# Kernel optimization log

Measured on AMD Instinct MI355X. Metric: run time of the kernel, lower is better.

The kernel has to match this reference:

```python
import jax, jax.numpy as jnp
import numpy as np

N_NODES = 50000
N_EDGES = 1600000
IN_FEATS = 256
OUT_FEATS = 64


def setup_inputs() -> dict:
    key = jax.random.key(0)
    k_x, k_w, k_b, k_s, k_d = jax.random.split(key, 5)
    x = jax.random.normal(k_x, (N_NODES, IN_FEATS), dtype=jnp.float32)
    # nn.Linear(in_feats, out_feats): weight [out, in], bias [out]
    W = jax.random.normal(k_w, (OUT_FEATS, IN_FEATS), dtype=jnp.float32) / np.sqrt(IN_FEATS)
    b = jax.random.normal(k_b, (OUT_FEATS,), dtype=jnp.float32) * 0.01
    edge_src = jax.random.randint(k_s, (N_EDGES,), 0, N_NODES, dtype=jnp.int32)
    edge_dst = jax.random.randint(k_d, (N_EDGES,), 0, N_NODES, dtype=jnp.int32)
    return {"x": x, "W": W, "b": b, "edge_src": edge_src, "edge_dst": edge_dst}


def reference(x, W, b, edge_src, edge_dst):
    # h = dropout(relu(Linear(x)))  -- dropout p=0 (eval) => identity
    h = jax.nn.relu(x @ W.T + b)                     # [N, out_feats]
    # update_all: message = h[src], reduce = mean over incoming edges per dst
    msg = h[edge_src]                                # [E, out_feats] gather
    summed = jax.ops.segment_sum(msg, edge_dst, num_segments=N_NODES)  # [N, out]
    deg = jax.ops.segment_sum(jnp.ones((edge_src.shape[0],), dtype=h.dtype),
                              edge_dst, num_segments=N_NODES)          # [N]
    deg = jnp.maximum(deg, 1.0)
    return summed / deg[:, None]
```

## Files before the change

### kernel.cpp

```cpp
#include <hip/hip_runtime.h>
#include <hip/hip_bf16.h>

#define K_IN 256
#define O_OUT 64
#define NBINS 1024
#define NPB 49
#define CAP 1824
#define PART_CHUNK 4096

typedef __attribute__((ext_vector_type(8))) short short8;
typedef __attribute__((ext_vector_type(4))) float f32x4;
typedef __attribute__((ext_vector_type(2))) unsigned u32x2;
typedef __attribute__((ext_vector_type(4))) unsigned u32x4;

#define GLOAD4(dst, base, voff, imm)                                     \
  asm volatile("global_load_dwordx4 %0, %1, %2 offset:" #imm             \
               : "=v"(dst) : "v"(voff), "s"(base))
#define GLOAD2(dst, base, voff)                                          \
  asm volatile("global_load_dwordx2 %0, %1, %2"                          \
               : "=v"(dst) : "v"(voff), "s"(base))
__device__ inline void vmwait0() {
  asm volatile("s_waitcnt vmcnt(0)" ::: "memory");
  __builtin_amdgcn_sched_barrier(0);
}

__device__ inline unsigned short bf16bits(float a) {
  __hip_bfloat16 t = __float2bfloat16(a);
  return *(unsigned short*)&t;
}

__device__ inline short8 cvt8u(u32x4 lo, u32x4 hi) {
  short8 r;
  r[0] = (short)bf16bits(__uint_as_float(lo[0]));
  r[1] = (short)bf16bits(__uint_as_float(lo[1]));
  r[2] = (short)bf16bits(__uint_as_float(lo[2]));
  r[3] = (short)bf16bits(__uint_as_float(lo[3]));
  r[4] = (short)bf16bits(__uint_as_float(hi[0]));
  r[5] = (short)bf16bits(__uint_as_float(hi[1]));
  r[6] = (short)bf16bits(__uint_as_float(hi[2]));
  r[7] = (short)bf16bits(__uint_as_float(hi[3]));
  return r;
}

__global__ __launch_bounds__(256) void k_prep(const float* __restrict__ W,
                                              unsigned short* __restrict__ Wb,
                                              int* __restrict__ cursor) {
  int i = blockIdx.x * 256 + threadIdx.x;
  Wb[i] = bf16bits(W[i]);
  if (i < NBINS) cursor[i] = 0;
}

struct GemmSmem {
  unsigned short wsb[64 * 256];
};
struct PartSmem {
  int cnt[NBINS];
  int scanb[NBINS];
  int gbase[NBINS];
  int wsum[4];
  unsigned ord[PART_CHUNK];
};
union FusedSmem {
  GemmSmem g;
  PartSmem p;
};

__device__ void gemm_body(GemmSmem& sm, int gid, const float* __restrict__ x,
                          const unsigned short* __restrict__ Wb,
                          const float* __restrict__ bias,
                          __hip_bfloat16* __restrict__ h, int N) {
  const int tid = threadIdx.x;
  const int lane = tid & 63;
  const int wv = tid >> 6;
  const int n0 = gid * 64;

  int anode = n0 + wv * 16 + (lane & 15);
  if (anode > N - 1) anode = N - 1;
  unsigned voff = (unsigned)anode * (K_IN * 4) + (unsigned)((lane >> 4) * 32);

  u32x4 f[16];
  GLOAD4(f[0], x, voff, 0);    GLOAD4(f[1], x, voff, 16);
  GLOAD4(f[2], x, voff, 128);  GLOAD4(f[3], x, voff, 144);
  GLOAD4(f[4], x, voff, 256);  GLOAD4(f[5], x, voff, 272);
  GLOAD4(f[6], x, voff, 384);  GLOAD4(f[7], x, voff, 400);
  GLOAD4(f[8], x, voff, 512);  GLOAD4(f[9], x, voff, 528);
  GLOAD4(f[10], x, voff, 640); GLOAD4(f[11], x, voff, 656);
  GLOAD4(f[12], x, voff, 768); GLOAD4(f[13], x, voff, 784);
  GLOAD4(f[14], x, voff, 896); GLOAD4(f[15], x, voff, 912);
  __builtin_amdgcn_sched_barrier(0);

  {
    const uint4* wsrc = (const uint4*)Wb;
#pragma unroll
    for (int r = 0; r < 8; ++r) {
      uint4 w = wsrc[r * 256 + tid];
      int flat = r * 256 + tid;
      int row = flat >> 5;
      int c16 = flat & 31;
      unsigned byte = (unsigned)(row * 512 + c16 * 16);
      byte ^= (unsigned)((row & 7) << 4);
      *(uint4*)((char*)sm.wsb + byte) = w;
    }
  }
  __syncthreads();
  vmwait0();

  const int brow0 = lane & 15;
  const unsigned kb = (unsigned)((lane >> 4) * 16);
  const unsigned bswz = (unsigned)((brow0 & 7) << 4);

  f32x4 acc[4] = {{0.f, 0.f, 0.f, 0.f}, {0.f, 0.f, 0.f, 0.f},
                  {0.f, 0.f, 0.f, 0.f}, {0.f, 0.f, 0.f, 0.f}};
#pragma unroll
  for (int k8 = 0; k8 < 8; ++k8) {
    short8 a = cvt8u(f[2 * k8], f[2 * k8 + 1]);
#pragma unroll
    for (int nt = 0; nt < 4; ++nt) {
      unsigned byte = (unsigned)((brow0 + nt * 16) * 512 + k8 * 64) + kb;
      byte ^= bswz;
      short8 bfr = *(const short8*)((const char*)sm.wsb + byte);
      acc[nt] = __builtin_amdgcn_mfma_f32_16x16x32_bf16(a, bfr, acc[nt], 0, 0, 0);
    }
  }

  const int col = lane & 15;
  const int rbase = (lane >> 4) * 4;
#pragma unroll
  for (int nt = 0; nt < 4; ++nt) {
    float bv = bias[nt * 16 + col];
#pragma unroll
    for (int j = 0; j < 4; ++j) {
      int node = n0 + wv * 16 + rbase + j;
      if (node < N) {
        float v = fmaxf(acc[nt][j] + bv, 0.f);
        h[(size_t)node * O_OUT + nt * 16 + col] = __float2bfloat16(v);
      }
    }
  }
}

__device__ void part_body(PartSmem& sm, int pid, const int* __restrict__ esrc,
                          const int* __restrict__ edst, int* __restrict__ cursor,
                          unsigned* __restrict__ bucket, int E) {
  const int tid = threadIdx.x;
  const int lane = tid & 63;
  const int wid = tid >> 6;
  const int base = pid * PART_CHUNK;

  u32x4 s4[4], d4[4];
  unsigned vo[4];
#pragma unroll
  for (int r = 0; r < 4; ++r) {
    int e0 = base + r * 1024 + tid * 4;
    if (e0 > E - 4) e0 = E - 4;
    vo[r] = (unsigned)e0 * 4u;
  }
  GLOAD4(s4[0], esrc, vo[0], 0); GLOAD4(d4[0], edst, vo[0], 0);
  GLOAD4(s4[1], esrc, vo[1], 0); GLOAD4(d4[1], edst, vo[1], 0);
  GLOAD4(s4[2], esrc, vo[2], 0); GLOAD4(d4[2], edst, vo[2], 0);
  GLOAD4(s4[3], esrc, vo[3], 0); GLOAD4(d4[3], edst, vo[3], 0);
  __builtin_amdgcn_sched_barrier(0);

#pragma unroll
  for (int r = 0; r < 4; ++r) sm.cnt[r * 256 + tid] = 0;
  __syncthreads();
  vmwait0();

  unsigned pk[16];
  int rk[16];
#pragma unroll
  for (int r = 0; r < 4; ++r) {
#pragma unroll
    for (int j = 0; j < 4; ++j) {
      int k = r * 4 + j;
      int e = base + r * 1024 + tid * 4 + j;
      if (e < E) {
        int d = (int)d4[r][j];
        int bb = (int)__umulhi((unsigned)d, 87652394u);
        int dl = d - bb * NPB;
        pk[k] = (s4[r][j] & 0xFFFFu) | ((unsigned)dl << 16) | ((unsigned)bb << 22);
        rk[k] = atomicAdd(&sm.cnt[bb], 1);
      } else {
        rk[k] = -1;
      }
    }
  }
  __syncthreads();

  int c0 = sm.cnt[4 * tid];
  int c1 = sm.cnt[4 * tid + 1];
  int c2 = sm.cnt[4 * tid + 2];
  int c3 = sm.cnt[4 * tid + 3];
  int s = c0 + c1 + c2 + c3;
  int incl = s;
#pragma unroll
  for (int off = 1; off < 64; off <<= 1) {
    int t = __shfl_up(incl, off);
    if (lane >= off) incl += t;
  }
  if (lane == 63) sm.wsum[wid] = incl;
  __syncthreads();
  int wpre = 0;
  for (int w = 0; w < wid; ++w) wpre += sm.wsum[w];
  int excl = wpre + incl - s;
  sm.scanb[4 * tid] = excl;
  sm.scanb[4 * tid + 1] = excl + c0;
  sm.scanb[4 * tid + 2] = excl + c0 + c1;
  sm.scanb[4 * tid + 3] = excl + c0 + c1 + c2;
  sm.gbase[4 * tid] = (c0 > 0) ? atomicAdd(&cursor[4 * tid], c0) : 0;
  sm.gbase[4 * tid + 1] = (c1 > 0) ? atomicAdd(&cursor[4 * tid + 1], c1) : 0;
  sm.gbase[4 * tid + 2] = (c2 > 0) ? atomicAdd(&cursor[4 * tid + 2], c2) : 0;
  sm.gbase[4 * tid + 3] = (c3 > 0) ? atomicAdd(&cursor[4 * tid + 3], c3) : 0;
  __syncthreads();

#pragma unroll
  for (int k = 0; k < 16; ++k) {
    if (rk[k] >= 0) {
      int bb = (int)(pk[k] >> 22);
      int pos = sm.scanb[bb] + rk[k];
      sm.ord[pos] = pk[k];
    }
  }
  __syncthreads();

  int nv = E - base;
  if (nv > PART_CHUNK) nv = PART_CHUNK;
  for (int p = tid; p < nv; p += 256) {
    unsigned v = sm.ord[p];
    int bb = v >> 22;
    int slot = sm.gbase[bb] + (p - sm.scanb[bb]);
    if (slot < CAP) bucket[(size_t)bb * CAP + slot] = v;
  }
}

__global__ __launch_bounds__(256, 4) void k_fused(const float* __restrict__ x,
                                                  const unsigned short* __restrict__ Wb,
                                                  const float* __restrict__ bias,
                                                  __hip_bfloat16* __restrict__ h,
                                                  const int* __restrict__ esrc,
                                                  const int* __restrict__ edst,
                                                  int* __restrict__ cursor,
                                                  unsigned* __restrict__ bucket,
                                                  int N, int E) {
  __shared__ FusedSmem sm;
  const int npart = (E + PART_CHUNK - 1) / PART_CHUNK;
  const int b = blockIdx.x;
  if (b % 3 == 1 && b / 3 < npart) {
    part_body(sm.p, b / 3, esrc, edst, cursor, bucket, E);
  } else {
    int skipped = (b + 2) / 3;
    if (skipped > npart) skipped = npart;
    gemm_body(sm.g, b - skipped, x, Wb, bias, h, N);
  }
}

__global__ __launch_bounds__(256, 4) void k_sortagg(const unsigned* __restrict__ bucket,
                                                    const int* __restrict__ cursor,
                                                    const unsigned* __restrict__ h32,
                                                    float* __restrict__ out, int N) {
  __shared__ int hist[NPB];
  __shared__ int offs[NPB];
  __shared__ unsigned short sbuf[CAP + 64];

  const int tid = threadIdx.x;
  const int lane = tid & 63;
  const int wid = tid >> 6;
  const int bin = blockIdx.x;

  if (tid < NPB) hist[tid] = 0;
  __syncthreads();

  int cnt = cursor[bin];
  if (cnt > CAP) cnt = CAP;
  const unsigned* bb = bucket + (size_t)bin * CAP;

  unsigned pk2[2][4];
  int rk2[2][4];
#pragma unroll
  for (int g = 0; g < 2; ++g) {
    int i0 = (g * 256 + tid) * 4;
    uint4 v;
    if (i0 + 3 < cnt) {
      v = *(const uint4*)(bb + i0);
    } else {
      v = make_uint4(0, 0, 0, 0);
      unsigned* vp = (unsigned*)&v;
      for (int j = 0; j < 4; ++j)
        if (i0 + j < cnt) vp[j] = bb[i0 + j];
    }
    const unsigned* vp = (const unsigned*)&v;
#pragma unroll
    for (int j = 0; j < 4; ++j) {
      if (i0 + j < cnt) {
        pk2[g][j] = vp[j];
        rk2[g][j] = atomicAdd(&hist[(vp[j] >> 16) & 63], 1);
      } else {
        rk2[g][j] = -1;
      }
    }
  }
  __syncthreads();

  if (tid < 64) {
    int hval = (tid < NPB) ? hist[tid] : 0;
    int incl = hval;
#pragma unroll
    for (int off = 1; off < 64; off <<= 1) {
      int t = __shfl_up(incl, off);
      if (lane >= off) incl += t;
    }
    if (tid < NPB) offs[tid] = incl - hval;
  }
  __syncthreads();

#pragma unroll
  for (int g = 0; g < 2; ++g)
#pragma unroll
    for (int j = 0; j < 4; ++j)
      if (rk2[g][j] >= 0)
        sbuf[offs[(pk2[g][j] >> 16) & 63] + rk2[g][j]] =
            (unsigned short)(pk2[g][j] & 0xFFFFu);
  __syncthreads();

  const int q = lane >> 4;
  const int hl = lane & 15;
  const unsigned hlb = (unsigned)hl * 8u;

  for (int nl = wid; nl < NPB; nl += 8) {
    const int nlb = nl + 4;
    const bool hasb = (nlb < NPB);
    const int ca = hist[nl];
    const int cb = hasb ? hist[nlb] : 0;
    const unsigned short* bsa = sbuf + offs[nl];
    const unsigned short* bsb = sbuf + (hasb ? offs[nlb] : 0);

    unsigned voa[12], vob[12];
#pragma unroll
    for (int k = 0; k < 12; ++k) {
      int e = k * 4 + q;
      unsigned pa = (e < ca) ? (unsigned)bsa[e] : 0u;
      unsigned pb = (e < cb) ? (unsigned)bsb[e] : 0u;
      voa[k] = pa * 128u + hlb;
      vob[k] = pb * 128u + hlb;
    }
    u32x2 ua[12], ub[12];
#pragma unroll
    for (int k = 0; k < 12; ++k) { GLOAD2(ua[k], h32, voa[k]); }
#pragma unroll
    for (int k = 0; k < 12; ++k) { GLOAD2(ub[k], h32, vob[k]); }
    vmwait0();

    float a0 = 0.f, a1 = 0.f, a2 = 0.f, a3 = 0.f;
    float b0 = 0.f, b1 = 0.f, b2 = 0.f, b3 = 0.f;
#pragma unroll
    for (int k = 0; k < 12; ++k) {
      float wk = (k * 4 + q < ca) ? 1.f : 0.f;
      a0 = fmaf(wk, __uint_as_float(ua[k][0] << 16), a0);
      a1 = fmaf(wk, __uint_as_float(ua[k][0] & 0xFFFF0000u), a1);
      a2 = fmaf(wk, __uint_as_float(ua[k][1] << 16), a2);
      a3 = fmaf(wk, __uint_as_float(ua[k][1] & 0xFFFF0000u), a3);
    }
#pragma unroll
    for (int k = 0; k < 12; ++k) {
      float wk = (k * 4 + q < cb) ? 1.f : 0.f;
      b0 = fmaf(wk, __uint_as_float(ub[k][0] << 16), b0);
      b1 = fmaf(wk, __uint_as_float(ub[k][0] & 0xFFFF0000u), b1);
      b2 = fmaf(wk, __uint_as_float(ub[k][1] << 16), b2);
      b3 = fmaf(wk, __uint_as_float(ub[k][1] & 0xFFFF0000u), b3);
    }

    const uint2* __restrict__ h2 = (const uint2*)h32;
    for (int e0 = 48; e0 < ca; e0 += 4) {
      int e = e0 + q;
      float wk = (e < ca) ? 1.f : 0.f;
      int p = (e < ca) ? (int)bsa[e] : 0;
      uint2 u = h2[(size_t)p * 16 + hl];
      a0 = fmaf(wk, __uint_as_float(u.x << 16), a0);
      a1 = fmaf(wk, __uint_as_float(u.x & 0xFFFF0000u), a1);
      a2 = fmaf(wk, __uint_as_float(u.y << 16), a2);
      a3 = fmaf(wk, __uint_as_float(u.y & 0xFFFF0000u), a3);
    }
    for (int e0 = 48; e0 < cb; e0 += 4) {
      int e = e0 + q;
      float wk = (e < cb) ? 1.f : 0.f;
      int p = (e < cb) ? (int)bsb[e] : 0;
      uint2 u = h2[(size_t)p * 16 + hl];
      b0 = fmaf(wk, __uint_as_float(u.x << 16), b0);
      b1 = fmaf(wk, __uint_as_float(u.x & 0xFFFF0000u), b1);
      b2 = fmaf(wk, __uint_as_float(u.y << 16), b2);
      b3 = fmaf(wk, __uint_as_float(u.y & 0xFFFF0000u), b3);
    }

    a0 += __shfl_xor(a0, 16); a1 += __shfl_xor(a1, 16);
    a2 += __shfl_xor(a2, 16); a3 += __shfl_xor(a3, 16);
    b0 += __shfl_xor(b0, 16); b1 += __shfl_xor(b1, 16);
    b2 += __shfl_xor(b2, 16); b3 += __shfl_xor(b3, 16);
    a0 += __shfl_xor(a0, 32); a1 += __shfl_xor(a1, 32);
    a2 += __shfl_xor(a2, 32); a3 += __shfl_xor(a3, 32);
    b0 += __shfl_xor(b0, 32); b1 += __shfl_xor(b1, 32);
    b2 += __shfl_xor(b2, 32); b3 += __shfl_xor(b3, 32);

    if (lane < 16) {
      int na = bin * NPB + nl;
      if (na < N) {
        float inv = 1.f / fmaxf((float)ca, 1.f);
        float4 r;
        r.x = a0 * inv; r.y = a1 * inv; r.z = a2 * inv; r.w = a3 * inv;
        *(float4*)(out + (size_t)na * O_OUT + hl * 4) = r;
      }
      int nb = bin * NPB + nlb;
      if (hasb && nb < N) {
        float inv = 1.f / fmaxf((float)cb, 1.f);
        float4 r;
        r.x = b0 * inv; r.y = b1 * inv; r.z = b2 * inv; r.w = b3 * inv;
        *(float4*)(out + (size_t)nb * O_OUT + hl * 4) = r;
      }
    }
  }
}

extern "C" void kernel_launch(void* const* d_in, const int* in_sizes, int n_in,
                              void* d_out, int out_size, void* d_ws, size_t ws_size,
                              hipStream_t stream) {
  const float* x = (const float*)d_in[0];
  const float* W = (const float*)d_in[1];
  const float* b = (const float*)d_in[2];
  const int* esrc = (const int*)d_in[3];
  const int* edst = (const int*)d_in[4];
  float* out = (float*)d_out;

  const int N = in_sizes[0] / K_IN;
  const int E = in_sizes[3];

  char* ws = (char*)d_ws;
  unsigned short* Wb = (unsigned short*)ws;
  __hip_bfloat16* h = (__hip_bfloat16*)(ws + 32768);
  size_t off = 32768 + (size_t)N * O_OUT * sizeof(__hip_bfloat16);
  int* cursor = (int*)(ws + off);
  off += NBINS * sizeof(int);
  unsigned* bucket = (unsigned*)(ws + off);

  const int ngemm = (N + 63) / 64;
  const int npart = (E + PART_CHUNK - 1) / PART_CHUNK;

  k_prep<<<(K_IN * O_OUT) / 256, 256, 0, stream>>>(W, Wb, cursor);
  k_fused<<<ngemm + npart, 256, 0, stream>>>(x, Wb, b, h, esrc, edst, cursor,
                                             bucket, N, E);
  k_sortagg<<<NBINS, 256, 0, stream>>>(bucket, cursor, (const unsigned*)h, out, N);
}
```

Measured before the change: 160.7 us.

## Shrink LDS use: GEMM reads W from global, halve partition chunk, raise occupancy

The GEMM path stops staging the bf16 weight matrix in LDS and reads B fragments straight from global/L2. It also drops the hand-issued asm loads in favour of plain float4 loads. The partition chunk is halved to 2048 edges and the count and scan arrays are merged, so the fused kernel's shared memory shrinks. Blocks now alternate strictly between GEMM and partition roles, and launch bounds ask for 8 blocks per CU. The aim is higher occupancy and better latency hiding, at the cost of repeated global reads of W, twice as many partition blocks, and more global cursor atomics.

```diff
diff --git a/kernel.cpp b/kernel.cpp
--- a/kernel.cpp
+++ b/kernel.cpp
@@ -6,16 +6,12 @@
 #define NBINS 1024
 #define NPB 49
 #define CAP 1824
-#define PART_CHUNK 4096
+#define PART_CHUNK 2048
 
 typedef __attribute__((ext_vector_type(8))) short short8;
 typedef __attribute__((ext_vector_type(4))) float f32x4;
 typedef __attribute__((ext_vector_type(2))) unsigned u32x2;
-typedef __attribute__((ext_vector_type(4))) unsigned u32x4;
-
-#define GLOAD4(dst, base, voff, imm)                                     \
-  asm volatile("global_load_dwordx4 %0, %1, %2 offset:" #imm             \
-               : "=v"(dst) : "v"(voff), "s"(base))
+
 #define GLOAD2(dst, base, voff)                                          \
   asm volatile("global_load_dwordx2 %0, %1, %2"                          \
                : "=v"(dst) : "v"(voff), "s"(base))
@@ -29,16 +25,12 @@
   return *(unsigned short*)&t;
 }
 
-__device__ inline short8 cvt8u(u32x4 lo, u32x4 hi) {
+__device__ inline short8 cvt8(float4 f0, float4 f1) {
   short8 r;
-  r[0] = (short)bf16bits(__uint_as_float(lo[0]));
-  r[1] = (short)bf16bits(__uint_as_float(lo[1]));
-  r[2] = (short)bf16bits(__uint_as_float(lo[2]));
-  r[3] = (short)bf16bits(__uint_as_float(lo[3]));
-  r[4] = (short)bf16bits(__uint_as_float(hi[0]));
-  r[5] = (short)bf16bits(__uint_as_float(hi[1]));
-  r[6] = (short)bf16bits(__uint_as_float(hi[2]));
-  r[7] = (short)bf16bits(__uint_as_float(hi[3]));
+  r[0] = (short)bf16bits(f0.x); r[1] = (short)bf16bits(f0.y);
+  r[2] = (short)bf16bits(f0.z); r[3] = (short)bf16bits(f0.w);
+  r[4] = (short)bf16bits(f1.x); r[5] = (short)bf16bits(f1.y);
+  r[6] = (short)bf16bits(f1.z); r[7] = (short)bf16bits(f1.w);
   return r;
 }
 
@@ -50,22 +42,14 @@
   if (i < NBINS) cursor[i] = 0;
 }
 
-struct GemmSmem {
-  unsigned short wsb[64 * 256];
-};
 struct PartSmem {
-  int cnt[NBINS];
-  int scanb[NBINS];
+  int cntscan[NBINS];
   int gbase[NBINS];
   int wsum[4];
   unsigned ord[PART_CHUNK];
 };
-union FusedSmem {
-  GemmSmem g;
-  PartSmem p;
-};
-
-__device__ void gemm_body(GemmSmem& sm, int gid, const float* __restrict__ x,
+
+__device__ void gemm_body(int gid, const float* __restrict__ x,
                           const unsigned short* __restrict__ Wb,
                           const float* __restrict__ bias,
                           __hip_bfloat16* __restrict__ h, int N) {
@@ -76,49 +60,19 @@
 
   int anode = n0 + wv * 16 + (lane & 15);
   if (anode > N - 1) anode = N - 1;
-  unsigned voff = (unsigned)anode * (K_IN * 4) + (unsigned)((lane >> 4) * 32);
-
-  u32x4 f[16];
-  GLOAD4(f[0], x, voff, 0);    GLOAD4(f[1], x, voff, 16);
-  GLOAD4(f[2], x, voff, 128);  GLOAD4(f[3], x, voff, 144);
-  GLOAD4(f[4], x, voff, 256);  GLOAD4(f[5], x, voff, 272);
-  GLOAD4(f[6], x, voff, 384);  GLOAD4(f[7], x, voff, 400);
-  GLOAD4(f[8], x, voff, 512);  GLOAD4(f[9], x, voff, 528);
-  GLOAD4(f[10], x, voff, 640); GLOAD4(f[11], x, voff, 656);
-  GLOAD4(f[12], x, voff, 768); GLOAD4(f[13], x, voff, 784);
-  GLOAD4(f[14], x, voff, 896); GLOAD4(f[15], x, voff, 912);
-  __builtin_amdgcn_sched_barrier(0);
-
-  {
-    const uint4* wsrc = (const uint4*)Wb;
-#pragma unroll
-    for (int r = 0; r < 8; ++r) {
-      uint4 w = wsrc[r * 256 + tid];
-      int flat = r * 256 + tid;
-      int row = flat >> 5;
-      int c16 = flat & 31;
-      unsigned byte = (unsigned)(row * 512 + c16 * 16);
-      byte ^= (unsigned)((row & 7) << 4);
-      *(uint4*)((char*)sm.wsb + byte) = w;
-    }
-  }
-  __syncthreads();
-  vmwait0();
-
-  const int brow0 = lane & 15;
-  const unsigned kb = (unsigned)((lane >> 4) * 16);
-  const unsigned bswz = (unsigned)((brow0 & 7) << 4);
+  const float* aptr = x + (size_t)anode * K_IN + (lane >> 4) * 8;
+  const unsigned short* bptr = Wb + (lane & 15) * K_IN + (lane >> 4) * 8;
 
   f32x4 acc[4] = {{0.f, 0.f, 0.f, 0.f}, {0.f, 0.f, 0.f, 0.f},
                   {0.f, 0.f, 0.f, 0.f}, {0.f, 0.f, 0.f, 0.f}};
 #pragma unroll
   for (int k8 = 0; k8 < 8; ++k8) {
-    short8 a = cvt8u(f[2 * k8], f[2 * k8 + 1]);
+    float4 f0 = *(const float4*)(aptr + k8 * 32);
+    float4 f1 = *(const float4*)(aptr + k8 * 32 + 4);
+    short8 a = cvt8(f0, f1);
 #pragma unroll
     for (int nt = 0; nt < 4; ++nt) {
-      unsigned byte = (unsigned)((brow0 + nt * 16) * 512 + k8 * 64) + kb;
-      byte ^= bswz;
-      short8 bfr = *(const short8*)((const char*)sm.wsb + byte);
+      short8 bfr = *(const short8*)(bptr + nt * 16 * K_IN + k8 * 32);
       acc[nt] = __builtin_amdgcn_mfma_f32_16x16x32_bf16(a, bfr, acc[nt], 0, 0, 0);
     }
   }
@@ -147,39 +101,36 @@
   const int wid = tid >> 6;
   const int base = pid * PART_CHUNK;
 
-  u32x4 s4[4], d4[4];
-  unsigned vo[4];
-#pragma unroll
-  for (int r = 0; r < 4; ++r) {
+#pragma unroll
+  for (int r = 0; r < 4; ++r) sm.cntscan[r * 256 + tid] = 0;
+
+  int4 s4[2], d4[2];
+#pragma unroll
+  for (int r = 0; r < 2; ++r) {
     int e0 = base + r * 1024 + tid * 4;
     if (e0 > E - 4) e0 = E - 4;
-    vo[r] = (unsigned)e0 * 4u;
-  }
-  GLOAD4(s4[0], esrc, vo[0], 0); GLOAD4(d4[0], edst, vo[0], 0);
-  GLOAD4(s4[1], esrc, vo[1], 0); GLOAD4(d4[1], edst, vo[1], 0);
-  GLOAD4(s4[2], esrc, vo[2], 0); GLOAD4(d4[2], edst, vo[2], 0);
-  GLOAD4(s4[3], esrc, vo[3], 0); GLOAD4(d4[3], edst, vo[3], 0);
-  __builtin_amdgcn_sched_barrier(0);
-
-#pragma unroll
-  for (int r = 0; r < 4; ++r) sm.cnt[r * 256 + tid] = 0;
-  __syncthreads();
-  vmwait0();
-
-  unsigned pk[16];
-  int rk[16];
-#pragma unroll
-  for (int r = 0; r < 4; ++r) {
+    s4[r] = *(const int4*)(esrc + e0);
+    d4[r] = *(const int4*)(edst + e0);
+  }
+  __syncthreads();
+
+  unsigned pk[8];
+  int rk[8];
+#pragma unroll
+  for (int r = 0; r < 2; ++r) {
+    const int* sp = (const int*)&s4[r];
+    const int* dp = (const int*)&d4[r];
 #pragma unroll
     for (int j = 0; j < 4; ++j) {
       int k = r * 4 + j;
       int e = base + r * 1024 + tid * 4 + j;
       if (e < E) {
-        int d = (int)d4[r][j];
+        int d = dp[j];
         int bb = (int)__umulhi((unsigned)d, 87652394u);
         int dl = d - bb * NPB;
-        pk[k] = (s4[r][j] & 0xFFFFu) | ((unsigned)dl << 16) | ((unsigned)bb << 22);
-        rk[k] = atomicAdd(&sm.cnt[bb], 1);
+        pk[k] = ((unsigned)sp[j] & 0xFFFFu) | ((unsigned)dl << 16) |
+                ((unsigned)bb << 22);
+        rk[k] = atomicAdd(&sm.cntscan[bb], 1);
       } else {
         rk[k] = -1;
       }
@@ -187,10 +138,10 @@
   }
   __syncthreads();
 
-  int c0 = sm.cnt[4 * tid];
-  int c1 = sm.cnt[4 * tid + 1];
-  int c2 = sm.cnt[4 * tid + 2];
-  int c3 = sm.cnt[4 * tid + 3];
+  int c0 = sm.cntscan[4 * tid];
+  int c1 = sm.cntscan[4 * tid + 1];
+  int c2 = sm.cntscan[4 * tid + 2];
+  int c3 = sm.cntscan[4 * tid + 3];
   int s = c0 + c1 + c2 + c3;
   int incl = s;
 #pragma unroll
@@ -203,10 +154,10 @@
   int wpre = 0;
   for (int w = 0; w < wid; ++w) wpre += sm.wsum[w];
   int excl = wpre + incl - s;
-  sm.scanb[4 * tid] = excl;
-  sm.scanb[4 * tid + 1] = excl + c0;
-  sm.scanb[4 * tid + 2] = excl + c0 + c1;
-  sm.scanb[4 * tid + 3] = excl + c0 + c1 + c2;
+  sm.cntscan[4 * tid] = excl;
+  sm.cntscan[4 * tid + 1] = excl + c0;
+  sm.cntscan[4 * tid + 2] = excl + c0 + c1;
+  sm.cntscan[4 * tid + 3] = excl + c0 + c1 + c2;
   sm.gbase[4 * tid] = (c0 > 0) ? atomicAdd(&cursor[4 * tid], c0) : 0;
   sm.gbase[4 * tid + 1] = (c1 > 0) ? atomicAdd(&cursor[4 * tid + 1], c1) : 0;
   sm.gbase[4 * tid + 2] = (c2 > 0) ? atomicAdd(&cursor[4 * tid + 2], c2) : 0;
@@ -214,11 +165,10 @@
   __syncthreads();
 
 #pragma unroll
-  for (int k = 0; k < 16; ++k) {
+  for (int k = 0; k < 8; ++k) {
     if (rk[k] >= 0) {
       int bb = (int)(pk[k] >> 22);
-      int pos = sm.scanb[bb] + rk[k];
-      sm.ord[pos] = pk[k];
+      sm.ord[sm.cntscan[bb] + rk[k]] = pk[k];
     }
   }
   __syncthreads();
@@ -228,12 +178,12 @@
   for (int p = tid; p < nv; p += 256) {
     unsigned v = sm.ord[p];
     int bb = v >> 22;
-    int slot = sm.gbase[bb] + (p - sm.scanb[bb]);
+    int slot = sm.gbase[bb] + (p - sm.cntscan[bb]);
     if (slot < CAP) bucket[(size_t)bb * CAP + slot] = v;
   }
 }
 
-__global__ __launch_bounds__(256, 4) void k_fused(const float* __restrict__ x,
+__global__ __launch_bounds__(256, 8) void k_fused(const float* __restrict__ x,
                                                   const unsigned short* __restrict__ Wb,
                                                   const float* __restrict__ bias,
                                                   __hip_bfloat16* __restrict__ h,
@@ -242,16 +192,10 @@
                                                   int* __restrict__ cursor,
                                                   unsigned* __restrict__ bucket,
                                                   int N, int E) {
-  __shared__ FusedSmem sm;
-  const int npart = (E + PART_CHUNK - 1) / PART_CHUNK;
+  __shared__ PartSmem sm;
   const int b = blockIdx.x;
-  if (b % 3 == 1 && b / 3 < npart) {
-    part_body(sm.p, b / 3, esrc, edst, cursor, bucket, E);
-  } else {
-    int skipped = (b + 2) / 3;
-    if (skipped > npart) skipped = npart;
-    gemm_body(sm.g, b - skipped, x, Wb, bias, h, N);
-  }
+  if (b & 1) part_body(sm, b >> 1, esrc, edst, cursor, bucket, E);
+  else gemm_body(b >> 1, x, Wb, bias, h, N);
 }
 
 __global__ __launch_bounds__(256, 4) void k_sortagg(const unsigned* __restrict__ bucket,
```

Result: slower. 189.6 us (+17.9%).

## Stage x tile through LDS as bf16 and drop inline-asm loads

Applied to the files above, without the earlier changes.

The GEMM part no longer keeps the whole x row fragment in 16 vector registers loaded by inline asm. It loads x cooperatively with coalesced float4 reads, converts to bf16, writes a swizzled tile into a new LDS buffer, and reads MFMA A-fragments from LDS. The partition part switches from asm loads to plain int4 loads with a scalar tail path. Launch bounds drop to 2 blocks per CU, and LDS per block doubles for the GEMM layout. Coalescing improves and register pressure falls, but occupancy drops and the early overlap of x loads with the W staging is lost.

```diff
diff --git a/kernel.cpp b/kernel.cpp
--- a/kernel.cpp
+++ b/kernel.cpp
@@ -11,11 +11,7 @@
 typedef __attribute__((ext_vector_type(8))) short short8;
 typedef __attribute__((ext_vector_type(4))) float f32x4;
 typedef __attribute__((ext_vector_type(2))) unsigned u32x2;
-typedef __attribute__((ext_vector_type(4))) unsigned u32x4;
-
-#define GLOAD4(dst, base, voff, imm)                                     \
-  asm volatile("global_load_dwordx4 %0, %1, %2 offset:" #imm             \
-               : "=v"(dst) : "v"(voff), "s"(base))
+
 #define GLOAD2(dst, base, voff)                                          \
   asm volatile("global_load_dwordx2 %0, %1, %2"                          \
                : "=v"(dst) : "v"(voff), "s"(base))
@@ -29,16 +25,12 @@
   return *(unsigned short*)&t;
 }
 
-__device__ inline short8 cvt8u(u32x4 lo, u32x4 hi) {
+__device__ inline short8 cvt8(float4 f0, float4 f1) {
   short8 r;
-  r[0] = (short)bf16bits(__uint_as_float(lo[0]));
-  r[1] = (short)bf16bits(__uint_as_float(lo[1]));
-  r[2] = (short)bf16bits(__uint_as_float(lo[2]));
-  r[3] = (short)bf16bits(__uint_as_float(lo[3]));
-  r[4] = (short)bf16bits(__uint_as_float(hi[0]));
-  r[5] = (short)bf16bits(__uint_as_float(hi[1]));
-  r[6] = (short)bf16bits(__uint_as_float(hi[2]));
-  r[7] = (short)bf16bits(__uint_as_float(hi[3]));
+  r[0] = (short)bf16bits(f0.x); r[1] = (short)bf16bits(f0.y);
+  r[2] = (short)bf16bits(f0.z); r[3] = (short)bf16bits(f0.w);
+  r[4] = (short)bf16bits(f1.x); r[5] = (short)bf16bits(f1.y);
+  r[6] = (short)bf16bits(f1.z); r[7] = (short)bf16bits(f1.w);
   return r;
 }
 
@@ -52,6 +44,7 @@
 
 struct GemmSmem {
   unsigned short wsb[64 * 256];
+  unsigned short xs[64 * 256];
 };
 struct PartSmem {
   int cnt[NBINS];
@@ -74,21 +67,6 @@
   const int wv = tid >> 6;
   const int n0 = gid * 64;
 
-  int anode = n0 + wv * 16 + (lane & 15);
-  if (anode > N - 1) anode = N - 1;
-  unsigned voff = (unsigned)anode * (K_IN * 4) + (unsigned)((lane >> 4) * 32);
-
-  u32x4 f[16];
-  GLOAD4(f[0], x, voff, 0);    GLOAD4(f[1], x, voff, 16);
-  GLOAD4(f[2], x, voff, 128);  GLOAD4(f[3], x, voff, 144);
-  GLOAD4(f[4], x, voff, 256);  GLOAD4(f[5], x, voff, 272);
-  GLOAD4(f[6], x, voff, 384);  GLOAD4(f[7], x, voff, 400);
-  GLOAD4(f[8], x, voff, 512);  GLOAD4(f[9], x, voff, 528);
-  GLOAD4(f[10], x, voff, 640); GLOAD4(f[11], x, voff, 656);
-  GLOAD4(f[12], x, voff, 768); GLOAD4(f[13], x, voff, 784);
-  GLOAD4(f[14], x, voff, 896); GLOAD4(f[15], x, voff, 912);
-  __builtin_amdgcn_sched_barrier(0);
-
   {
     const uint4* wsrc = (const uint4*)Wb;
 #pragma unroll
@@ -102,18 +80,38 @@
       *(uint4*)((char*)sm.wsb + byte) = w;
     }
   }
-  __syncthreads();
-  vmwait0();
+
+  {
+#pragma unroll
+    for (int r = 0; r < 8; ++r) {
+      int c = r * 256 + tid;
+      int row = c >> 5;
+      int c16 = c & 31;
+      int node = n0 + row;
+      if (node > N - 1) node = N - 1;
+      const float4* ps = (const float4*)(x + (size_t)node * K_IN + c16 * 8);
+      float4 f0 = ps[0];
+      float4 f1 = ps[1];
+      unsigned byte = (unsigned)(row * 512 + c16 * 16);
+      byte ^= (unsigned)((row & 7) << 4);
+      *(short8*)((char*)sm.xs + byte) = cvt8(f0, f1);
+    }
+  }
+  __syncthreads();
 
   const int brow0 = lane & 15;
   const unsigned kb = (unsigned)((lane >> 4) * 16);
   const unsigned bswz = (unsigned)((brow0 & 7) << 4);
+  const int arow = wv * 16 + (lane & 15);
+  const unsigned aswz = (unsigned)((arow & 7) << 4);
+  const unsigned abase = (unsigned)(arow * 512) + kb;
 
   f32x4 acc[4] = {{0.f, 0.f, 0.f, 0.f}, {0.f, 0.f, 0.f, 0.f},
                   {0.f, 0.f, 0.f, 0.f}, {0.f, 0.f, 0.f, 0.f}};
 #pragma unroll
   for (int k8 = 0; k8 < 8; ++k8) {
-    short8 a = cvt8u(f[2 * k8], f[2 * k8 + 1]);
+    unsigned ab = (abase + (unsigned)(k8 * 64)) ^ aswz;
+    short8 a = *(const short8*)((const char*)sm.xs + ab);
 #pragma unroll
     for (int nt = 0; nt < 4; ++nt) {
       unsigned byte = (unsigned)((brow0 + nt * 16) * 512 + k8 * 64) + kb;
@@ -147,38 +145,43 @@
   const int wid = tid >> 6;
   const int base = pid * PART_CHUNK;
 
-  u32x4 s4[4], d4[4];
-  unsigned vo[4];
+#pragma unroll
+  for (int r = 0; r < 4; ++r) sm.cnt[r * 256 + tid] = 0;
+
+  int4 s4[4], d4[4];
 #pragma unroll
   for (int r = 0; r < 4; ++r) {
     int e0 = base + r * 1024 + tid * 4;
-    if (e0 > E - 4) e0 = E - 4;
-    vo[r] = (unsigned)e0 * 4u;
-  }
-  GLOAD4(s4[0], esrc, vo[0], 0); GLOAD4(d4[0], edst, vo[0], 0);
-  GLOAD4(s4[1], esrc, vo[1], 0); GLOAD4(d4[1], edst, vo[1], 0);
-  GLOAD4(s4[2], esrc, vo[2], 0); GLOAD4(d4[2], edst, vo[2], 0);
-  GLOAD4(s4[3], esrc, vo[3], 0); GLOAD4(d4[3], edst, vo[3], 0);
-  __builtin_amdgcn_sched_barrier(0);
-
-#pragma unroll
-  for (int r = 0; r < 4; ++r) sm.cnt[r * 256 + tid] = 0;
-  __syncthreads();
-  vmwait0();
+    if (e0 + 3 < E) {
+      s4[r] = *(const int4*)(esrc + e0);
+      d4[r] = *(const int4*)(edst + e0);
+    } else {
+      s4[r] = make_int4(0, 0, 0, 0);
+      d4[r] = make_int4(0, 0, 0, 0);
+      int* sp = (int*)&s4[r];
+      int* dp = (int*)&d4[r];
+      for (int j = 0; j < 4; ++j)
+        if (e0 + j < E) { sp[j] = esrc[e0 + j]; dp[j] = edst[e0 + j]; }
+    }
+  }
+  __syncthreads();
 
   unsigned pk[16];
   int rk[16];
 #pragma unroll
   for (int r = 0; r < 4; ++r) {
+    const int* sp = (const int*)&s4[r];
+    const int* dp = (const int*)&d4[r];
 #pragma unroll
     for (int j = 0; j < 4; ++j) {
       int k = r * 4 + j;
       int e = base + r * 1024 + tid * 4 + j;
       if (e < E) {
-        int d = (int)d4[r][j];
+        int d = dp[j];
         int bb = (int)__umulhi((unsigned)d, 87652394u);
         int dl = d - bb * NPB;
-        pk[k] = (s4[r][j] & 0xFFFFu) | ((unsigned)dl << 16) | ((unsigned)bb << 22);
+        pk[k] = ((unsigned)sp[j] & 0xFFFFu) | ((unsigned)dl << 16) |
+                ((unsigned)bb << 22);
         rk[k] = atomicAdd(&sm.cnt[bb], 1);
       } else {
         rk[k] = -1;
@@ -217,8 +220,7 @@
   for (int k = 0; k < 16; ++k) {
     if (rk[k] >= 0) {
       int bb = (int)(pk[k] >> 22);
-      int pos = sm.scanb[bb] + rk[k];
-      sm.ord[pos] = pk[k];
+      sm.ord[sm.scanb[bb] + rk[k]] = pk[k];
     }
   }
   __syncthreads();
@@ -233,7 +235,7 @@
   }
 }
 
-__global__ __launch_bounds__(256, 4) void k_fused(const float* __restrict__ x,
+__global__ __launch_bounds__(256, 2) void k_fused(const float* __restrict__ x,
                                                   const unsigned short* __restrict__ Wb,
                                                   const float* __restrict__ bias,
                                                   __hip_bfloat16* __restrict__ h,
```

Result: slower. 165.2 us (+2.8%).
